# Optimization experiments

Hardware: AMD Instinct MI355X
Metric: run time of the kernel (lower is better)

The kernel has to match this reference:

```python
import jax, jax.numpy as jnp
import numpy as np

EPS = 1e-8
LAMB = 0.5
L2_NORM = 1e-4
NUM_USERS = 100000
NUM_ITEMS = 50000
EMBED = 64
R = 3
NNZ = 1_000_000
IG_NNZ = 500_000
B = 512
K = 100


def _spmm(rows, cols, vals, X, num_rows):
    # sparse [num_rows, n] @ X  via gather + segment-sum
    return jax.ops.segment_sum(X[cols] * vals[:, None], rows, num_segments=num_rows)


def setup_inputs() -> dict:
    key = jax.random.key(0)
    ks = jax.random.split(key, 16)
    user = jax.random.randint(ks[0], (B,), 0, NUM_USERS)
    item = jax.random.randint(ks[1], (B, K), 0, NUM_ITEMS)
    rel_rows = jax.random.randint(ks[2], (R, NNZ), 0, NUM_USERS)
    rel_cols = jax.random.randint(ks[3], (R, NNZ), 0, NUM_ITEMS)
    ig_rows = jax.random.randint(ks[4], (R, IG_NNZ), 0, NUM_ITEMS)
    ig_cols = jax.random.randint(ks[5], (R, IG_NNZ), 0, NUM_ITEMS)
    ig_vals = jnp.ones((R, IG_NNZ), jnp.float32)
    train_rows = jax.random.randint(ks[6], (NNZ,), 0, NUM_USERS)
    train_cols = jax.random.randint(ks[7], (NNZ,), 0, NUM_ITEMS)
    user_embedding = 0.1 * jax.random.normal(ks[8], (NUM_USERS, EMBED), jnp.float32)
    item_embedding = 0.1 * jax.random.normal(ks[9], (NUM_ITEMS, EMBED), jnp.float32)
    mgnn_weight = jnp.ones((R,), jnp.float32)
    item_behavior_W = 0.05 * jax.random.normal(ks[10], (R, 2 * EMBED, 2 * EMBED), jnp.float32)
    item_propagate_W = 0.05 * jax.random.normal(ks[11], (R, EMBED, EMBED), jnp.float32)
    W = 0.05 * jax.random.normal(ks[12], (EMBED, EMBED), jnp.float32)
    return {"user": user, "item": item, "rel_rows": rel_rows, "rel_cols": rel_cols,
            "ig_rows": ig_rows, "ig_cols": ig_cols, "ig_vals": ig_vals,
            "train_rows": train_rows, "train_cols": train_cols,
            "user_embedding": user_embedding, "item_embedding": item_embedding,
            "mgnn_weight": mgnn_weight, "item_behavior_W": item_behavior_W,
            "item_propagate_W": item_propagate_W, "W": W}


def reference(user, item, rel_rows, rel_cols, ig_rows, ig_cols, ig_vals,
              train_rows, train_cols, user_embedding, item_embedding,
              mgnn_weight, item_behavior_W, item_propagate_W, W):
    # user behavior degree [U, R] (number of interactions per user per relation)
    ub_deg = jax.vmap(lambda r: jax.ops.segment_sum(
        jnp.ones(r.shape, jnp.float32), r, num_segments=NUM_USERS))(rel_rows).T
    total_weight = ub_deg @ mgnn_weight[:, None]                       # [U,1]
    user_behavior_weight = ub_deg * mgnn_weight[None, :] / (total_weight + EPS)

    user_feature = jnp.zeros((NUM_USERS, EMBED), user_embedding.dtype)
    score2 = jnp.zeros((item.shape[0], item.shape[1]), user_embedding.dtype)
    for i in range(R):
        # item-item propagation for relation i
        ig_deg = jax.ops.segment_sum(ig_vals[i], ig_rows[i], num_segments=NUM_ITEMS)[:, None]
        item_agg = _spmm(ig_rows[i], ig_cols[i], ig_vals[i], item_embedding, NUM_ITEMS)
        item_agg = item_agg / (ig_deg + EPS)
        tmp_item_prop = jnp.concatenate([item_embedding, item_agg @ item_propagate_W[i]], axis=1)  # [I,2E]

        ones = jnp.ones(rel_rows[i].shape, user_embedding.dtype)
        ub_d = ub_deg[:, i:i + 1]
        tmp_user_neigh = _spmm(rel_rows[i], rel_cols[i], ones, item_embedding, NUM_USERS) / (ub_d + EPS)
        tmp_user_item_p = _spmm(rel_rows[i], rel_cols[i], ones, tmp_item_prop, NUM_USERS) / (ub_d + EPS)

        user_feature = user_feature + user_behavior_weight[:, i:i + 1] * tmp_user_neigh
        proj = tmp_user_item_p @ item_behavior_W[i]                    # [U,2E]
        # score2 term: <proj[user], tmp_item_prop[item]> per candidate
        score2 = score2 + jnp.einsum('be,bke->bk', proj[user], tmp_item_prop[item])
    score2 = score2 / R

    # item feature from transposed train matrix (values=1, no node dropout)
    item_feature = jax.ops.segment_sum(user_embedding[train_rows], train_cols, num_segments=NUM_ITEMS)

    uf = jnp.concatenate([user_embedding, user_feature @ W], axis=1)   # [U,2E]
    itf = jnp.concatenate([item_embedding, item_feature @ W], axis=1)  # [I,2E]

    u_g = uf[user]                                                     # [B,2E]
    i_g = itf[item]                                                    # [B,K,2E]
    score1 = jnp.einsum('be,bke->bk', u_g, i_g)
    scores = score1 + LAMB * score2
    # L2 on expanded user feature [B,K,2E] and gathered item feature
    l2_loss = L2_NORM * (item.shape[1] * (u_g ** 2).sum() + (i_g ** 2).sum())
    return scores, l2_loss
```

## Files before the change

kernel.cpp:

```cpp
#include <hip/hip_runtime.h>

#define EPSF     1e-8f
#define LAMBF    0.5f
#define L2NORMF  1e-4f
#define NUSERS   100000
#define NITEMS   50000
#define EMB      64
#define RREL     3
#define NNZ_     1000000
#define IGNNZ    500000
#define BB       512
#define KK       100

#define IGTOT    (RREL * IGNNZ)
#define TOTE     (IGTOT + NNZ_)
#define NBIN_SEG 782
#define NBINS    (4 * NBIN_SEG)
#define NBLK     128
#define BTH      1024
#define SLICE    ((TOTE + NBLK - 1) / NBLK)
#define CAPE     2048
#define GTH      512

__global__ void scatter_maps(const int* __restrict__ user, const int* __restrict__ item,
                             int* __restrict__ slot, int* __restrict__ iflag) {
    int i = blockIdx.x * blockDim.x + threadIdx.x;
    if (i < BB) slot[user[i]] = i;
    if (i < BB * KK) iflag[item[i]] = 1;
}

__device__ __forceinline__ int edge_bin(int i, const int* ig_rows, const int* train_cols) {
    if (i < IGTOT) return (i / IGNNZ) * NBIN_SEG + (ig_rows[i] >> 6);
    return 3 * NBIN_SEG + (train_cols[i - IGTOT] >> 6);
}

__global__ void pass1_count(const int* __restrict__ ig_rows, const int* __restrict__ train_cols,
                            int* __restrict__ pcnt) {
    __shared__ int h[NBINS];
    int b = blockIdx.x, t = threadIdx.x;
    for (int i = t; i < NBINS; i += BTH) h[i] = 0;
    __syncthreads();
    int s = b * SLICE, e = min(s + SLICE, TOTE);
    for (int i = s + t; i < e; i += BTH)
        atomicAdd(&h[edge_bin(i, ig_rows, train_cols)], 1);
    __syncthreads();
    for (int i = t; i < NBINS; i += BTH) pcnt[b * NBINS + i] = h[i];
}

__global__ void scan_tot(const int* __restrict__ pcnt, int* __restrict__ tot) {
    int bin = blockIdx.x * blockDim.x + threadIdx.x;
    if (bin >= NBINS) return;
    int s = 0;
    for (int b = 0; b < NBLK; b++) s += pcnt[b * NBINS + bin];
    tot[bin] = s;
}

__global__ void scan_bins(const int* __restrict__ tot, int* __restrict__ binbase) {
    __shared__ int csum[1024];
    int t = threadIdx.x;
    int base = t * 4;
    int v0 = (base + 0 < NBINS) ? tot[base + 0] : 0;
    int v1 = (base + 1 < NBINS) ? tot[base + 1] : 0;
    int v2 = (base + 2 < NBINS) ? tot[base + 2] : 0;
    int v3 = (base + 3 < NBINS) ? tot[base + 3] : 0;
    int s = v0 + v1 + v2 + v3;
    csum[t] = s;
    __syncthreads();
    for (int d = 1; d < 1024; d <<= 1) {
        int x = (t >= d) ? csum[t - d] : 0;
        __syncthreads();
        csum[t] += x;
        __syncthreads();
    }
    int run = csum[t] - s;
    if (base + 0 < NBINS) { binbase[base + 0] = run; run += v0; }
    if (base + 1 < NBINS) { binbase[base + 1] = run; run += v1; }
    if (base + 2 < NBINS) { binbase[base + 2] = run; run += v2; }
    if (base + 3 < NBINS) { binbase[base + 3] = run; run += v3; }
    if (t == 0) binbase[NBINS] = TOTE;
}

__global__ void scan_obase(const int* __restrict__ pcnt, const int* __restrict__ binbase,
                           int* __restrict__ obase) {
    int bin = blockIdx.x * blockDim.x + threadIdx.x;
    if (bin >= NBINS) return;
    int run = binbase[bin];
    for (int b = 0; b < NBLK; b++) {
        obase[b * NBINS + bin] = run;
        run += pcnt[b * NBINS + bin];
    }
}

__global__ void pass2_scatter(const int* __restrict__ ig_rows, const int* __restrict__ ig_cols,
                              const float* __restrict__ ig_vals, const int* __restrict__ train_rows,
                              const int* __restrict__ train_cols, const int* __restrict__ obase,
                              int2* __restrict__ garr, int* __restrict__ tcol) {
    __shared__ int pos[NBINS];
    int b = blockIdx.x, t = threadIdx.x;
    for (int i = t; i < NBINS; i += BTH) pos[i] = obase[b * NBINS + i];
    __syncthreads();
    int s = b * SLICE, e = min(s + SLICE, TOTE);
    for (int i = s + t; i < e; i += BTH) {
        if (i < IGTOT) {
            int dest = ig_rows[i];
            int bin = (i / IGNNZ) * NBIN_SEG + (dest >> 6);
            int slot = atomicAdd(&pos[bin], 1);
            garr[slot] = make_int2((ig_cols[i] << 6) | (dest & 63),
                                   __float_as_int(ig_vals[i]));
        } else {
            int e2 = i - IGTOT;
            int dest = train_cols[e2];
            int bin = 3 * NBIN_SEG + (dest >> 6);
            int slot = atomicAdd(&pos[bin], 1);
            tcol[slot - IGTOT] = (train_rows[e2] << 6) | (dest & 63);
        }
    }
}

__global__ void ig_bin_gather(const float* __restrict__ item_emb, const int* __restrict__ binbase,
                              const int2* __restrict__ garr, const float* __restrict__ Wp,
                              float* __restrict__ prop2, int seg) {
    __shared__ int scol[CAPE];
    __shared__ float sval[CAPE];
    __shared__ int cnt[64], off[65], pos[64];
    int t = threadIdx.x, w = t >> 6, lane = t & 63;
    int bin = seg * NBIN_SEG + blockIdx.x;
    int bstart = binbase[bin], bend = binbase[bin + 1];
    int n = bend - bstart;
    int row0 = blockIdx.x * 64;
    if (n <= CAPE) {
        if (t < 64) cnt[t] = 0;
        __syncthreads();
        for (int i = t; i < n; i += GTH) atomicAdd(&cnt[garr[bstart + i].x & 63], 1);
        __syncthreads();
        if (t == 0) {
            int run = 0;
            for (int j = 0; j < 64; j++) { off[j] = run; run += cnt[j]; }
            off[64] = run;
        }
        __syncthreads();
        if (t < 64) pos[t] = off[t];
        __syncthreads();
        for (int i = t; i < n; i += GTH) {
            int2 pv = garr[bstart + i];
            int sl = atomicAdd(&pos[pv.x & 63], 1);
            scol[sl] = pv.x >> 6;
            sval[sl] = __int_as_float(pv.y);
        }
        __syncthreads();
        for (int r = w; r < 64; r += 8) {
            int grow = row0 + r;
            if (grow >= NITEMS) break;
            int s = off[r], e = off[r + 1];
            float acc = 0.f, deg = 0.f;
            for (int k = s; k < e; k += 8) {
                int i0 = min(k + 0, e - 1), i1 = min(k + 1, e - 1);
                int i2 = min(k + 2, e - 1), i3 = min(k + 3, e - 1);
                int i4 = min(k + 4, e - 1), i5 = min(k + 5, e - 1);
                int i6 = min(k + 6, e - 1), i7 = min(k + 7, e - 1);
                int c0 = scol[i0], c1 = scol[i1], c2 = scol[i2], c3 = scol[i3];
                int c4 = scol[i4], c5 = scol[i5], c6 = scol[i6], c7 = scol[i7];
                float v0 = (k + 0 < e) ? sval[i0] : 0.f, v1 = (k + 1 < e) ? sval[i1] : 0.f;
                float v2 = (k + 2 < e) ? sval[i2] : 0.f, v3 = (k + 3 < e) ? sval[i3] : 0.f;
                float v4 = (k + 4 < e) ? sval[i4] : 0.f, v5 = (k + 5 < e) ? sval[i5] : 0.f;
                float v6 = (k + 6 < e) ? sval[i6] : 0.f, v7 = (k + 7 < e) ? sval[i7] : 0.f;
                float f0 = item_emb[c0 * 64 + lane], f1 = item_emb[c1 * 64 + lane];
                float f2 = item_emb[c2 * 64 + lane], f3 = item_emb[c3 * 64 + lane];
                float f4 = item_emb[c4 * 64 + lane], f5 = item_emb[c5 * 64 + lane];
                float f6 = item_emb[c6 * 64 + lane], f7 = item_emb[c7 * 64 + lane];
                acc += v0 * f0 + v1 * f1 + v2 * f2 + v3 * f3
                     + v4 * f4 + v5 * f5 + v6 * f6 + v7 * f7;
                deg += (v0 + v1 + v2 + v3) + (v4 + v5 + v6 + v7);
            }
            float av = acc / (deg + EPSF);
            float o = 0.f;
#pragma unroll 8
            for (int k2 = 0; k2 < 64; k2++) o += __shfl(av, k2) * Wp[k2 * 64 + lane];
            prop2[grow * 64 + lane] = o;
        }
    } else {
        for (int r = w; r < 64; r += 8) {
            int grow = row0 + r;
            if (grow >= NITEMS) break;
            float acc = 0.f, deg = 0.f;
            for (int j0 = bstart; j0 < bend; j0 += 64) {
                int j = j0 + lane;
                int2 pv = (j < bend) ? garr[j] : make_int2(-1, 0);
                unsigned long long mask = __ballot(pv.x >= 0 && (pv.x & 63) == r);
                while (mask) {
                    int jj = __builtin_ctzll(mask); mask &= mask - 1;
                    int pj = __shfl(pv.x, jj);
                    float vj = __shfl(__int_as_float(pv.y), jj);
                    acc += vj * item_emb[(pj >> 6) * 64 + lane];
                    deg += vj;
                }
            }
            float av = acc / (deg + EPSF);
            float o = 0.f;
#pragma unroll 8
            for (int k2 = 0; k2 < 64; k2++) o += __shfl(av, k2) * Wp[k2 * 64 + lane];
            prop2[grow * 64 + lane] = o;
        }
    }
}

__global__ void train_bin_gather(const float* __restrict__ user_emb, const int* __restrict__ binbase,
                                 const int* __restrict__ tcol, const int* __restrict__ iflag,
                                 const float* __restrict__ Wm, float* __restrict__ itf2) {
    __shared__ int scol[CAPE];
    __shared__ int cnt[64], off[65], pos[64];
    int t = threadIdx.x, w = t >> 6, lane = t & 63;
    int bin = 3 * NBIN_SEG + blockIdx.x;
    int bstart = binbase[bin] - IGTOT, bend = binbase[bin + 1] - IGTOT;
    int n = bend - bstart;
    int row0 = blockIdx.x * 64;
    if (n <= CAPE) {
        if (t < 64) cnt[t] = 0;
        __syncthreads();
        for (int i = t; i < n; i += GTH) atomicAdd(&cnt[tcol[bstart + i] & 63], 1);
        __syncthreads();
        if (t == 0) {
            int run = 0;
            for (int j = 0; j < 64; j++) { off[j] = run; run += cnt[j]; }
            off[64] = run;
        }
        __syncthreads();
        if (t < 64) pos[t] = off[t];
        __syncthreads();
        for (int i = t; i < n; i += GTH) {
            int p = tcol[bstart + i];
            int sl = atomicAdd(&pos[p & 63], 1);
            scol[sl] = p >> 6;
        }
        __syncthreads();
        for (int r = w; r < 64; r += 8) {
            int grow = row0 + r;
            if (grow >= NITEMS) break;
            if (!iflag[grow]) continue;
            int s = off[r], e = off[r + 1];
            float acc = 0.f;
            for (int k = s; k < e; k += 8) {
                int i0 = min(k + 0, e - 1), i1 = min(k + 1, e - 1);
                int i2 = min(k + 2, e - 1), i3 = min(k + 3, e - 1);
                int i4 = min(k + 4, e - 1), i5 = min(k + 5, e - 1);
                int i6 = min(k + 6, e - 1), i7 = min(k + 7, e - 1);
                int c0 = scol[i0], c1 = scol[i1], c2 = scol[i2], c3 = scol[i3];
                int c4 = scol[i4], c5 = scol[i5], c6 = scol[i6], c7 = scol[i7];
                float m1 = (k + 1 < e) ? 1.f : 0.f, m2 = (k + 2 < e) ? 1.f : 0.f;
                float m3 = (k + 3 < e) ? 1.f : 0.f, m4 = (k + 4 < e) ? 1.f : 0.f;
                float m5 = (k + 5 < e) ? 1.f : 0.f, m6 = (k + 6 < e) ? 1.f : 0.f;
                float m7 = (k + 7 < e) ? 1.f : 0.f;
                float f0 = user_emb[c0 * 64 + lane], f1 = user_emb[c1 * 64 + lane];
                float f2 = user_emb[c2 * 64 + lane], f3 = user_emb[c3 * 64 + lane];
                float f4 = user_emb[c4 * 64 + lane], f5 = user_emb[c5 * 64 + lane];
                float f6 = user_emb[c6 * 64 + lane], f7 = user_emb[c7 * 64 + lane];
                acc += f0 + m1 * f1 + m2 * f2 + m3 * f3
                     + m4 * f4 + m5 * f5 + m6 * f6 + m7 * f7;
            }
            float o = 0.f;
#pragma unroll 8
            for (int k2 = 0; k2 < 64; k2++) o += __shfl(acc, k2) * Wm[k2 * 64 + lane];
            itf2[grow * 64 + lane] = o;
        }
    } else {
        for (int r = w; r < 64; r += 8) {
            int grow = row0 + r;
            if (grow >= NITEMS) break;
            if (!iflag[grow]) continue;
            float acc = 0.f;
            for (int j0 = bstart; j0 < bend; j0 += 64) {
                int j = j0 + lane;
                int p = (j < bend) ? tcol[j] : -1;
                unsigned long long mask = __ballot(p >= 0 && (p & 63) == r);
                while (mask) {
                    int jj = __builtin_ctzll(mask); mask &= mask - 1;
                    int pj = __shfl(p, jj);
                    acc += user_emb[(pj >> 6) * 64 + lane];
                }
            }
            float o = 0.f;
#pragma unroll 8
            for (int k2 = 0; k2 < 64; k2++) o += __shfl(acc, k2) * Wm[k2 * 64 + lane];
            itf2[grow * 64 + lane] = o;
        }
    }
}

__device__ __forceinline__ void rel_hit(int s, int c, int lane,
                                        const float* __restrict__ item_emb,
                                        const float* __restrict__ prop2,
                                        float* __restrict__ accN, float* __restrict__ accP,
                                        float* __restrict__ ubc) {
    unsigned long long mask = __ballot(s >= 0);
    while (mask) {
        int j = __builtin_ctzll(mask);
        mask &= mask - 1;
        int bs = __shfl(s, j);
        int bc = __shfl(c, j);
        atomicAdd(&accN[bs * EMB + lane], item_emb[bc * EMB + lane]);
        atomicAdd(&accP[bs * EMB + lane], prop2[bc * EMB + lane]);
        if (lane == 0) atomicAdd(&ubc[bs], 1.0f);
    }
}

__global__ void rel_scan(const int* __restrict__ rows, const int* __restrict__ cols,
                         const int* __restrict__ slot, const float* __restrict__ item_emb,
                         const float* __restrict__ prop2,
                         float* __restrict__ accN, float* __restrict__ accP,
                         float* __restrict__ ubc) {
    int lane = threadIdx.x & 63;
    int gw = (blockIdx.x * blockDim.x + threadIdx.x) >> 6;
    int nw = (gridDim.x * blockDim.x) >> 6;
    for (int ch = gw; ch < NNZ_ / 256; ch += nw) {
        int base = ch * 256 + lane * 4;
        int4 r4 = *reinterpret_cast<const int4*>(rows + base);
        int4 c4 = *reinterpret_cast<const int4*>(cols + base);
        int s0 = slot[r4.x], s1 = slot[r4.y], s2 = slot[r4.z], s3 = slot[r4.w];
        rel_hit(s0, c4.x, lane, item_emb, prop2, accN, accP, ubc);
        rel_hit(s1, c4.y, lane, item_emb, prop2, accN, accP, ubc);
        rel_hit(s2, c4.z, lane, item_emb, prop2, accN, accP, ubc);
        rel_hit(s3, c4.w, lane, item_emb, prop2, accN, accP, ubc);
    }
}

__global__ void proj_score2(const int* __restrict__ user, const int* __restrict__ slot,
                            const float* __restrict__ ubc, const float* __restrict__ acc_neigh,
                            const float* __restrict__ acc_prop, const float* __restrict__ Wb,
                            const int* __restrict__ item, const float* __restrict__ item_emb,
                            const float* __restrict__ item_prop2, float* __restrict__ score2) {
    int b = blockIdx.x;
    int tid = threadIdx.x;
    __shared__ float tbuf[128];
    __shared__ float p[128];
    int rep = slot[user[b]];
    float inv = 1.0f / (ubc[rep] + EPSF);
    if (tid < 64)       tbuf[tid] = acc_neigh[rep * 64 + tid] * inv;
    else if (tid < 128) tbuf[tid] = acc_prop[rep * 64 + (tid - 64)] * inv;
    __syncthreads();
    if (tid < 128) {
        float o = 0.f;
#pragma unroll 8
        for (int k = 0; k < 128; k++) o += tbuf[k] * Wb[k * 128 + tid];
        p[tid] = o;
    }
    __syncthreads();
    int wave = tid >> 6, lane = tid & 63;
    for (int k = wave; k < KK; k += 4) {
        int it = item[b * KK + k];
        float s = p[lane] * item_emb[it * 64 + lane] + p[64 + lane] * item_prop2[it * 64 + lane];
        for (int off = 32; off > 0; off >>= 1) s += __shfl_xor(s, off);
        if (lane == 0) score2[b * KK + k] += s;
    }
}

__global__ void final_k(const int* __restrict__ user, const int* __restrict__ item,
                        const int* __restrict__ slot, const float* __restrict__ ubc,
                        const float* __restrict__ acc_neigh, const float* __restrict__ mw,
                        const float* __restrict__ W, const float* __restrict__ user_emb,
                        const float* __restrict__ item_emb, const float* __restrict__ itf2,
                        const float* __restrict__ score2, float* __restrict__ out,
                        float* __restrict__ l2out) {
    int b = blockIdx.x;
    int tid = threadIdx.x;
    int wave = tid >> 6, lane = tid & 63;
    __shared__ float uf[64], u1[64], u2[64];
    __shared__ float red[4];
    int u = user[b];
    if (tid < 64) {
        int rep = slot[u];
        float w0 = mw[0], w1 = mw[1], w2 = mw[2];
        float c0 = ubc[0 * BB + rep], c1 = ubc[1 * BB + rep], c2 = ubc[2 * BB + rep];
        float invT = 1.0f / (c0 * w0 + c1 * w1 + c2 * w2 + EPSF);
        float f = (c0 * w0 * invT) / (c0 + EPSF) * acc_neigh[(0 * BB + rep) * 64 + tid]
                + (c1 * w1 * invT) / (c1 + EPSF) * acc_neigh[(1 * BB + rep) * 64 + tid]
                + (c2 * w2 * invT) / (c2 + EPSF) * acc_neigh[(2 * BB + rep) * 64 + tid];
        uf[tid] = f;
        u1[tid] = user_emb[u * 64 + tid];
    }
    __syncthreads();
    if (tid < 64) {
        float o = 0.f;
#pragma unroll
        for (int k = 0; k < 64; k++) o += uf[k] * W[k * 64 + tid];
        u2[tid] = o;
    }
    __syncthreads();
    float l2part = 0.f;
    for (int k = wave; k < KK; k += 4) {
        int it = item[b * KK + k];
        float e1 = item_emb[it * 64 + lane], e2 = itf2[it * 64 + lane];
        float s = u1[lane] * e1 + u2[lane] * e2;
        float q = e1 * e1 + e2 * e2;
        for (int off = 32; off > 0; off >>= 1) {
            s += __shfl_xor(s, off);
            q += __shfl_xor(q, off);
        }
        if (lane == 0) {
            out[b * KK + k] = s + LAMBF * (score2[b * KK + k] * (1.0f / (float)RREL));
            l2part += q;
        }
    }
    float su = u1[lane] * u1[lane] + u2[lane] * u2[lane];
    for (int off = 32; off > 0; off >>= 1) su += __shfl_xor(su, off);
    if (wave == 0 && lane == 0) l2part += (float)KK * su;
    if (lane == 0) red[wave] = l2part;
    __syncthreads();
    if (tid == 0) atomicAdd(l2out, L2NORMF * (red[0] + red[1] + red[2] + red[3]));
}

extern "C" void kernel_launch(void* const* d_in, const int* in_sizes, int n_in,
                              void* d_out, int out_size, void* d_ws, size_t ws_size,
                              hipStream_t stream) {
    const int*   user       = (const int*)d_in[0];
    const int*   item       = (const int*)d_in[1];
    const int*   rel_rows   = (const int*)d_in[2];
    const int*   rel_cols   = (const int*)d_in[3];
    const int*   ig_rows    = (const int*)d_in[4];
    const int*   ig_cols    = (const int*)d_in[5];
    const float* ig_vals    = (const float*)d_in[6];
    const int*   train_rows = (const int*)d_in[7];
    const int*   train_cols = (const int*)d_in[8];
    const float* user_emb   = (const float*)d_in[9];
    const float* item_emb   = (const float*)d_in[10];
    const float* mw         = (const float*)d_in[11];
    const float* Wb         = (const float*)d_in[12];
    const float* Wp         = (const float*)d_in[13];
    const float* W          = (const float*)d_in[14];
    float* out = (float*)d_out;

    float* ws = (float*)d_ws;
    size_t o = 0;
    int2*  garr       = (int2*)(ws + o); o += (size_t)IGTOT * 2;
    int*   tcol       = (int*)(ws + o); o += NNZ_;
    int*   user_slot  = (int*)(ws + o); o += NUSERS;
    int*   iflag      = (int*)(ws + o); o += NITEMS;
    int*   pcnt       = (int*)(ws + o); o += (size_t)NBLK * NBINS;
    int*   tot        = (int*)(ws + o); o += NBINS;
    int*   binbase    = (int*)(ws + o); o += NBINS + 1;
    int*   obase      = (int*)(ws + o); o += (size_t)NBLK * NBINS;
    float* item_prop2 = ws + o; o += (size_t)NITEMS * 64;
    float* acc_neigh  = ws + o; o += (size_t)RREL * BB * 64;
    float* acc_prop   = ws + o; o += (size_t)RREL * BB * 64;
    float* ubc        = ws + o; o += (size_t)RREL * BB;
    float* score2     = ws + o; o += (size_t)BB * KK;
    if (ws_size < o * sizeof(float)) return;

    size_t zero_zone = (size_t)RREL * BB * 64 * 2 + RREL * BB + BB * KK;

    hipMemsetAsync(user_slot, 0xFF, (size_t)NUSERS * 4, stream);
    hipMemsetAsync(iflag, 0, (size_t)NITEMS * 4, stream);
    hipMemsetAsync(acc_neigh, 0, zero_zone * 4, stream);
    hipMemsetAsync(out + (out_size - 1), 0, 4, stream);
    scatter_maps<<<(BB * KK + 255) / 256, 256, 0, stream>>>(user, item, user_slot, iflag);

    pass1_count<<<NBLK, BTH, 0, stream>>>(ig_rows, train_cols, pcnt);
    scan_tot<<<(NBINS + 255) / 256, 256, 0, stream>>>(pcnt, tot);
    scan_bins<<<1, 1024, 0, stream>>>(tot, binbase);
    scan_obase<<<(NBINS + 255) / 256, 256, 0, stream>>>(pcnt, binbase, obase);
    pass2_scatter<<<NBLK, BTH, 0, stream>>>(ig_rows, ig_cols, ig_vals, train_rows, train_cols,
                                            obase, garr, tcol);

    for (int i = 0; i < RREL; i++) {
        ig_bin_gather<<<NBIN_SEG, GTH, 0, stream>>>(item_emb, binbase, garr,
                                                    Wp + (size_t)i * 64 * 64, item_prop2, i);
        rel_scan<<<1024, 256, 0, stream>>>(rel_rows + (size_t)i * NNZ_, rel_cols + (size_t)i * NNZ_,
                                           user_slot, item_emb, item_prop2,
                                           acc_neigh + (size_t)i * BB * 64,
                                           acc_prop + (size_t)i * BB * 64, ubc + (size_t)i * BB);
        proj_score2<<<BB, 256, 0, stream>>>(user, user_slot, ubc + (size_t)i * BB,
                                            acc_neigh + (size_t)i * BB * 64,
                                            acc_prop + (size_t)i * BB * 64,
                                            Wb + (size_t)i * 128 * 128,
                                            item, item_emb, item_prop2, score2);
    }

    float* itf2 = item_prop2;
    train_bin_gather<<<NBIN_SEG, GTH, 0, stream>>>(user_emb, binbase, tcol, iflag, W, itf2);
    final_k<<<BB, 256, 0, stream>>>(user, item, user_slot, ubc, acc_neigh, mw, W,
                                    user_emb, item_emb, itf2, score2,
                                    out, out + (out_size - 1));
}
```

Measured before the change: 632.4 us.

## Split 64x64 weight projection into separate kernel and parallelize bin prefix scan

Removes the per-row shuffle-based 64x64 matvec from the bin-gather kernels and applies the weight projection in a new apply_w kernel that stages W in shared memory, reading and writing the rows in place. It also replaces the serial single-thread 64-entry prefix sum with a wave shuffle scan, which drops one barrier. The unfusion adds four extra launches and an extra read/write pass over the 50000x64 buffers. In exchange, the gather kernels get shorter critical paths and lower register pressure.

After: 592.9 us. -6.2%, faster.

```diff
diff --git a/kernel.cpp b/kernel.cpp
--- a/kernel.cpp
+++ b/kernel.cpp
@@ -117,9 +117,23 @@
     }
 }
 
+__device__ __forceinline__ void bin_scan(int t, int* cnt, int* off, int* pos) {
+    if (t < 64) {
+        int v = cnt[t];
+        int inc = v;
+#pragma unroll
+        for (int d = 1; d < 64; d <<= 1) {
+            int x = __shfl_up(inc, d);
+            if (t >= d) inc += x;
+        }
+        off[t] = inc - v;
+        pos[t] = inc - v;
+        if (t == 63) off[64] = inc;
+    }
+}
+
 __global__ void ig_bin_gather(const float* __restrict__ item_emb, const int* __restrict__ binbase,
-                              const int2* __restrict__ garr, const float* __restrict__ Wp,
-                              float* __restrict__ prop2, int seg) {
+                              const int2* __restrict__ garr, float* __restrict__ prop2, int seg) {
     __shared__ int scol[CAPE];
     __shared__ float sval[CAPE];
     __shared__ int cnt[64], off[65], pos[64];
@@ -133,13 +147,7 @@
         __syncthreads();
         for (int i = t; i < n; i += GTH) atomicAdd(&cnt[garr[bstart + i].x & 63], 1);
         __syncthreads();
-        if (t == 0) {
-            int run = 0;
-            for (int j = 0; j < 64; j++) { off[j] = run; run += cnt[j]; }
-            off[64] = run;
-        }
-        __syncthreads();
-        if (t < 64) pos[t] = off[t];
+        bin_scan(t, cnt, off, pos);
         __syncthreads();
         for (int i = t; i < n; i += GTH) {
             int2 pv = garr[bstart + i];
@@ -172,11 +180,7 @@
                      + v4 * f4 + v5 * f5 + v6 * f6 + v7 * f7;
                 deg += (v0 + v1 + v2 + v3) + (v4 + v5 + v6 + v7);
             }
-            float av = acc / (deg + EPSF);
-            float o = 0.f;
-#pragma unroll 8
-            for (int k2 = 0; k2 < 64; k2++) o += __shfl(av, k2) * Wp[k2 * 64 + lane];
-            prop2[grow * 64 + lane] = o;
+            prop2[grow * 64 + lane] = acc / (deg + EPSF);
         }
     } else {
         for (int r = w; r < 64; r += 8) {
@@ -195,18 +199,14 @@
                     deg += vj;
                 }
             }
-            float av = acc / (deg + EPSF);
-            float o = 0.f;
-#pragma unroll 8
-            for (int k2 = 0; k2 < 64; k2++) o += __shfl(av, k2) * Wp[k2 * 64 + lane];
-            prop2[grow * 64 + lane] = o;
+            prop2[grow * 64 + lane] = acc / (deg + EPSF);
         }
     }
 }
 
 __global__ void train_bin_gather(const float* __restrict__ user_emb, const int* __restrict__ binbase,
                                  const int* __restrict__ tcol, const int* __restrict__ iflag,
-                                 const float* __restrict__ Wm, float* __restrict__ itf2) {
+                                 float* __restrict__ itf2) {
     __shared__ int scol[CAPE];
     __shared__ int cnt[64], off[65], pos[64];
     int t = threadIdx.x, w = t >> 6, lane = t & 63;
@@ -219,13 +219,7 @@
         __syncthreads();
         for (int i = t; i < n; i += GTH) atomicAdd(&cnt[tcol[bstart + i] & 63], 1);
         __syncthreads();
-        if (t == 0) {
-            int run = 0;
-            for (int j = 0; j < 64; j++) { off[j] = run; run += cnt[j]; }
-            off[64] = run;
-        }
-        __syncthreads();
-        if (t < 64) pos[t] = off[t];
+        bin_scan(t, cnt, off, pos);
         __syncthreads();
         for (int i = t; i < n; i += GTH) {
             int p = tcol[bstart + i];
@@ -257,10 +251,7 @@
                 acc += f0 + m1 * f1 + m2 * f2 + m3 * f3
                      + m4 * f4 + m5 * f5 + m6 * f6 + m7 * f7;
             }
-            float o = 0.f;
-#pragma unroll 8
-            for (int k2 = 0; k2 < 64; k2++) o += __shfl(acc, k2) * Wm[k2 * 64 + lane];
-            itf2[grow * 64 + lane] = o;
+            itf2[grow * 64 + lane] = acc;
         }
     } else {
         for (int r = w; r < 64; r += 8) {
@@ -278,11 +269,27 @@
                     acc += user_emb[(pj >> 6) * 64 + lane];
                 }
             }
-            float o = 0.f;
-#pragma unroll 8
-            for (int k2 = 0; k2 < 64; k2++) o += __shfl(acc, k2) * Wm[k2 * 64 + lane];
-            itf2[grow * 64 + lane] = o;
-        }
+            itf2[grow * 64 + lane] = acc;
+        }
+    }
+}
+
+__global__ void apply_w(float* __restrict__ A, const float* __restrict__ Wm,
+                        const int* __restrict__ flag, int M) {
+    __shared__ float sW[64 * 64];
+    __shared__ float sA[4][64];
+    int tid = threadIdx.x;
+    for (int i = tid; i < 64 * 64; i += 256) sW[i] = Wm[i];
+    int lr = tid >> 6, c = tid & 63;
+    int row = blockIdx.x * 4 + lr;
+    bool act = (row < M) && (!flag || flag[row]);
+    if (act) sA[lr][c] = A[row * 64 + c];
+    __syncthreads();
+    if (act) {
+        float o = 0.f;
+#pragma unroll
+        for (int k = 0; k < 64; k++) o += sA[lr][k] * sW[k * 64 + c];
+        A[row * 64 + c] = o;
     }
 }
 
@@ -461,8 +468,9 @@
                                             obase, garr, tcol);
 
     for (int i = 0; i < RREL; i++) {
-        ig_bin_gather<<<NBIN_SEG, GTH, 0, stream>>>(item_emb, binbase, garr,
-                                                    Wp + (size_t)i * 64 * 64, item_prop2, i);
+        ig_bin_gather<<<NBIN_SEG, GTH, 0, stream>>>(item_emb, binbase, garr, item_prop2, i);
+        apply_w<<<(NITEMS + 3) / 4, 256, 0, stream>>>(item_prop2, Wp + (size_t)i * 64 * 64,
+                                                      nullptr, NITEMS);
         rel_scan<<<1024, 256, 0, stream>>>(rel_rows + (size_t)i * NNZ_, rel_cols + (size_t)i * NNZ_,
                                            user_slot, item_emb, item_prop2,
                                            acc_neigh + (size_t)i * BB * 64,
@@ -475,7 +483,8 @@
     }
 
     float* itf2 = item_prop2;
-    train_bin_gather<<<NBIN_SEG, GTH, 0, stream>>>(user_emb, binbase, tcol, iflag, W, itf2);
+    train_bin_gather<<<NBIN_SEG, GTH, 0, stream>>>(user_emb, binbase, tcol, iflag, itf2);
+    apply_w<<<(NITEMS + 3) / 4, 256, 0, stream>>>(itf2, W, iflag, NITEMS);
     final_k<<<BB, 256, 0, stream>>>(user, item, user_slot, ubc, acc_neigh, mw, W,
                                     user_emb, item_emb, itf2, score2,
                                     out, out + (out_size - 1));
```
